# Kernel tuning notes

Hardware: AMD Instinct MI355X
Metric: run time of the kernel (lower is better)

Reference implementation:

```python
import jax, jax.numpy as jnp
import numpy as np

N = 50000
LAMBDA_MAX = 2.0  # PyG default for sym normalization
EPS = 1e-5


def _edge_norm(src, dst, num_nodes):
    # PyG ChebConv.__norm__ with normalization='sym', edge_weight=None:
    # remove self loops, L = I - D^{-1/2} A D^{-1/2}, scale 2/lambda_max, add -1 self loops.
    w = jnp.where(src != dst, 1.0, 0.0)  # remove self loops
    deg = jax.ops.segment_sum(w, src, num_segments=num_nodes)
    dinv = jnp.where(deg > 0, jax.lax.rsqrt(jnp.maximum(deg, 1e-12)), 0.0)
    w_norm = -(2.0 / LAMBDA_MAX) * dinv[src] * w * dinv[dst]  # off-diagonal of scaled L
    diag = (2.0 / LAMBDA_MAX) * 1.0 - 1.0  # scalar diagonal (0.0 when lambda_max=2)
    return w_norm, diag


def _cheb_conv(x, src, dst, w_norm, diag, Ws, b, num_nodes):
    # out = sum_k T_k(L_hat) x @ W_k + b, via Chebyshev recurrence.
    def prop(h):
        msg = w_norm[:, None] * h[src]                       # [E, d]
        return jax.ops.segment_sum(msg, dst, num_segments=num_nodes) + diag * h

    K = Ws.shape[0]
    Tx0 = x
    out = Tx0 @ Ws[0]
    Tx1 = prop(x)
    out = out + Tx1 @ Ws[1]
    for k in range(2, K):
        Tx2 = 2.0 * prop(Tx1) - Tx0
        out = out + Tx2 @ Ws[k]
        Tx0, Tx1 = Tx1, Tx2
    return out + b


def _layernorm(h, g, bt):
    mu = jnp.mean(h, axis=-1, keepdims=True)
    var = jnp.mean(jnp.square(h - mu), axis=-1, keepdims=True)
    return (h - mu) * jax.lax.rsqrt(var + EPS) * g + bt


def setup_inputs() -> dict:
    key = jax.random.key(0)
    ks = jax.random.split(key, 4)
    x = jax.random.normal(ks[0], (N, 128), dtype=jnp.float32)
    edge_index = jax.random.randint(ks[1], (2, 800000), 0, N, dtype=jnp.int64)
    W1 = jax.random.normal(ks[2], (3, 128, 256), dtype=jnp.float32) * 0.05
    W2 = jax.random.normal(ks[3], (3, 256, 128), dtype=jnp.float32) * 0.05
    return {
        "x": x, "edge_index": edge_index,
        "W1": W1, "b1": jnp.zeros((256,), jnp.float32),
        "g1": jnp.ones((256,), jnp.float32), "bt1": jnp.zeros((256,), jnp.float32),
        "W2": W2, "b2": jnp.zeros((128,), jnp.float32),
        "g2": jnp.ones((128,), jnp.float32), "bt2": jnp.zeros((128,), jnp.float32),
    }


def reference(x, edge_index, W1, b1, g1, bt1, W2, b2, g2, bt2):
    src, dst = edge_index[0], edge_index[1]
    w_norm, diag = _edge_norm(src, dst, N)
    h = _cheb_conv(x, src, dst, w_norm, diag, W1, b1, N)
    h = jax.nn.relu(_layernorm(h, g1, bt1))  # dropout p=0 / eval -> identity
    h = _cheb_conv(h, src, dst, w_norm, diag, W2, b2, N)
    h = jax.nn.relu(_layernorm(h, g2, bt2))
    return h
```

## Files before the change

kernel.cpp:

```cpp
#include <hip/hip_runtime.h>

#define N_NODES 50000
#define NRANGE 8
#define RNG 6400
#define TOTR (NRANGE * RNG)
#define NCHUNK 32

using f32x4  = __attribute__((ext_vector_type(4))) float;
using bf16x8 = __attribute__((ext_vector_type(8))) __bf16;

__device__ __forceinline__ unsigned short f2bf(float f) {
    unsigned int b = __float_as_uint(f);
    unsigned int r = (b + 0x7FFFu + ((b >> 16) & 1u)) >> 16;
    return (unsigned short)r;
}
__device__ __forceinline__ float bf_lo(unsigned int u) { return __uint_as_float(u << 16); }
__device__ __forceinline__ float bf_hi(unsigned int u) { return __uint_as_float(u & 0xFFFF0000u); }
__device__ __forceinline__ unsigned int packbf(float x, float y) {
    return ((unsigned int)f2bf(y) << 16) | f2bf(x);
}


__global__ void cvt_bf_kernel(const float* __restrict__ in, unsigned short* __restrict__ out, size_t n4) {
    size_t i = (size_t)blockIdx.x * blockDim.x + threadIdx.x;
    if (i < n4) {
        float4 v = *reinterpret_cast<const float4*>(in + i * 4);
        ushort4 o;
        o.x = f2bf(v.x); o.y = f2bf(v.y); o.z = f2bf(v.z); o.w = f2bf(v.w);
        *reinterpret_cast<ushort4*>(out + i * 4) = o;
    }
}

__global__ void wtrans1_kernel(const float* __restrict__ W, unsigned short* __restrict__ Bt) {
    int i = blockIdx.x * blockDim.x + threadIdx.x;
    if (i < 3 * 128 * 256) {
        int c = i % 256;
        int kg = i / 256;
        Bt[(size_t)c * 384 + kg] = f2bf(W[(size_t)kg * 256 + c]);
    }
}

__global__ void wtrans2_kernel(const float* __restrict__ W, unsigned short* __restrict__ Btc) {
    int i = blockIdx.x * blockDim.x + threadIdx.x;
    if (i < 384 * 256) {
        int k = i % 256;
        int cc = i / 256;
        int seg = cc >> 7, c = cc & 127;
        float v;
        if (seg == 0)      v = W[(size_t)k * 128 + c] - W[(size_t)(2 * 256 + k) * 128 + c];
        else if (seg == 1) v = W[(size_t)(256 + k) * 128 + c];
        else               v = 2.0f * W[(size_t)(2 * 256 + k) * 128 + c];
        Btc[(size_t)cc * 256 + k] = f2bf(v);
    }
}


__global__ __launch_bounds__(1024) void hist_priv_kernel(
        const int* __restrict__ src, const int* __restrict__ dst, int E, int chunk,
        int* __restrict__ pd, int* __restrict__ pc) {
    __shared__ int lhS[RNG];
    __shared__ int lhD[RNG];
    int r = blockIdx.x & (NRANGE - 1);
    int c = blockIdx.x >> 3;
    int lo = r * RNG;
    for (int i = threadIdx.x; i < RNG; i += 1024) { lhS[i] = 0; lhD[i] = 0; }
    __syncthreads();
    int e0 = c * chunk, e1 = min(e0 + chunk, E);
    for (int e = e0 + threadIdx.x; e < e1; e += 1024) {
        int s = src[e], d = dst[e];
        if (s != d) {
            unsigned int sr = (unsigned int)(s - lo);
            unsigned int dr = (unsigned int)(d - lo);
            if (sr < RNG) atomicAdd(&lhS[sr], 1);
            if (dr < RNG) atomicAdd(&lhD[dr], 1);
        }
    }
    __syncthreads();
    int base = c * TOTR + lo;
    for (int i = threadIdx.x; i < RNG; i += 1024) {
        pd[base + i] = lhS[i];
        pc[base + i] = lhD[i];
    }
}

__global__ void reduce_chunks_kernel(int* __restrict__ pd, int* __restrict__ pc,
                                     float* __restrict__ dinv, int* __restrict__ cnt, int n) {
    int i = blockIdx.x * blockDim.x + threadIdx.x;
    if (i >= TOTR) return;
    int degs = 0;
#pragma unroll 8
    for (int c = 0; c < NCHUNK; ++c) degs += pd[c * TOTR + i];
    int run = 0;
#pragma unroll 8
    for (int c = 0; c < NCHUNK; ++c) {
        int v = pc[c * TOTR + i];
        pc[c * TOTR + i] = run;
        run += v;
    }
    if (i < n) {
        dinv[i] = degs > 0 ? rsqrtf((float)degs) : 0.0f;
        cnt[i] = run;
    }
}


__global__ __launch_bounds__(1024) void scan1_kernel(const int* __restrict__ cnt,
                                                     int* __restrict__ excl,
                                                     int* __restrict__ bsum, int n) {
    __shared__ int wsum[16];
    int tid = threadIdx.x, lane = tid & 63, wid = tid >> 6;
    int i = blockIdx.x * 1024 + tid;
    int v = (i < n) ? cnt[i] : 0;
    int x = v;
#pragma unroll
    for (int o = 1; o < 64; o <<= 1) { int y = __shfl_up(x, o); if (lane >= o) x += y; }
    if (lane == 63) wsum[wid] = x;
    __syncthreads();
    if (tid < 16) {
        int s = wsum[tid];
#pragma unroll
        for (int o = 1; o < 16; o <<= 1) { int y = __shfl_up(s, o); if (tid >= o) s += y; }
        wsum[tid] = s;
    }
    __syncthreads();
    int base = (wid > 0 ? wsum[wid - 1] : 0);
    if (i < n) excl[i] = base + x - v;
    if (tid == 0) bsum[blockIdx.x] = wsum[15];
}

__global__ void scan2_kernel(int* __restrict__ bsum, int nb) {
    int t = threadIdx.x;
    int v = (t < nb) ? bsum[t] : 0;
    int x = v;
#pragma unroll
    for (int o = 1; o < 64; o <<= 1) { int y = __shfl_up(x, o); if (t >= o) x += y; }
    if (t < nb) bsum[t] = x - v;
}

__global__ __launch_bounds__(1024) void scan3_kernel(const int* __restrict__ excl,
                                                     const int* __restrict__ bsum,
                                                     const int* __restrict__ cnt,
                                                     int* __restrict__ rowptr, int n) {
    int i = blockIdx.x * 1024 + threadIdx.x;
    if (i < n) {
        int rp = excl[i] + bsum[blockIdx.x];
        rowptr[i] = rp;
        if (i == n - 1) rowptr[n] = rp + cnt[i];
    }
}

__global__ __launch_bounds__(1024) void csr_place_kernel(
        const int* __restrict__ src, const int* __restrict__ dst, int E, int chunk,
        const int* __restrict__ pc, const int* __restrict__ rowptr,
        const float* __restrict__ dinv,
        int* __restrict__ csr_src, float* __restrict__ csr_w, int n) {
    __shared__ int cur[RNG];
    __shared__ float dloc[RNG];
    int r = blockIdx.x & (NRANGE - 1);
    int c = blockIdx.x >> 3;
    int lo = r * RNG;
    for (int i = threadIdx.x; i < RNG; i += 1024) {
        int node = lo + i;
        if (node < n) {
            cur[i] = rowptr[node] + pc[c * TOTR + node];
            dloc[i] = dinv[node];
        }
    }
    __syncthreads();
    int e0 = c * chunk, e1 = min(e0 + chunk, E);
    for (int e = e0 + threadIdx.x; e < e1; e += 1024) {
        int s = src[e], d = dst[e];
        unsigned int dr = (unsigned int)(d - lo);
        if (s != d && dr < RNG) {
            int pos = atomicAdd(&cur[dr], 1);
            csr_src[pos] = s;
            csr_w[pos] = -dinv[s] * dloc[dr];
        }
    }
}


__global__ void prop_kernel(const unsigned int* __restrict__ H, int hs,
                            const int* __restrict__ rowptr,
                            const int* __restrict__ csr_src,
                            const float* __restrict__ csr_w,
                            const unsigned int* __restrict__ add, int as_,
                            float scale, float coef,
                            unsigned int* __restrict__ out, int n) {
    int wib = threadIdx.x >> 6;
    int lane = threadIdx.x & 63;
    int node = blockIdx.x * (blockDim.x >> 6) + wib;
    if (node >= n) return;

    float ax = 0.0f, ay = 0.0f;
    int beg = rowptr[node], end = rowptr[node + 1];
    int i = beg;
    for (; i + 4 <= end; i += 4) {
        int s0 = csr_src[i], s1 = csr_src[i + 1], s2 = csr_src[i + 2], s3 = csr_src[i + 3];
        float w0 = csr_w[i], w1 = csr_w[i + 1], w2 = csr_w[i + 2], w3 = csr_w[i + 3];
        unsigned int u0 = H[(size_t)s0 * hs + lane];
        unsigned int u1 = H[(size_t)s1 * hs + lane];
        unsigned int u2 = H[(size_t)s2 * hs + lane];
        unsigned int u3 = H[(size_t)s3 * hs + lane];
        ax += w0 * bf_lo(u0) + w1 * bf_lo(u1) + w2 * bf_lo(u2) + w3 * bf_lo(u3);
        ay += w0 * bf_hi(u0) + w1 * bf_hi(u1) + w2 * bf_hi(u2) + w3 * bf_hi(u3);
    }
    for (; i < end; ++i) {
        int s0 = csr_src[i];
        float w0 = csr_w[i];
        unsigned int u0 = H[(size_t)s0 * hs + lane];
        ax += w0 * bf_lo(u0);
        ay += w0 * bf_hi(u0);
    }

    float vx = scale * ax, vy = scale * ay;
    if (add) {
        unsigned int au = add[(size_t)node * as_ + lane];
        vx += coef * bf_lo(au);
        vy += coef * bf_hi(au);
    }
    out[(size_t)node * 64 + lane] = packbf(vx, vy);
}

__global__ void prop_ln_kernel(const unsigned int* __restrict__ V,
                               const int* __restrict__ rowptr,
                               const int* __restrict__ csr_src,
                               const float* __restrict__ csr_w,
                               const unsigned int* __restrict__ U0,
                               const float* __restrict__ b,
                               const float* __restrict__ g,
                               const float* __restrict__ bt,
                               float* __restrict__ out, int n) {
    int wib = threadIdx.x >> 6;
    int lane = threadIdx.x & 63;
    int node = blockIdx.x * (blockDim.x >> 6) + wib;
    if (node >= n) return;

    float ax = 0.0f, ay = 0.0f;
    int beg = rowptr[node], end = rowptr[node + 1];
    int i = beg;
    for (; i + 4 <= end; i += 4) {
        int s0 = csr_src[i], s1 = csr_src[i + 1], s2 = csr_src[i + 2], s3 = csr_src[i + 3];
        float w0 = csr_w[i], w1 = csr_w[i + 1], w2 = csr_w[i + 2], w3 = csr_w[i + 3];
        unsigned int u0 = V[(size_t)s0 * 64 + lane];
        unsigned int u1 = V[(size_t)s1 * 64 + lane];
        unsigned int u2 = V[(size_t)s2 * 64 + lane];
        unsigned int u3 = V[(size_t)s3 * 64 + lane];
        ax += w0 * bf_lo(u0) + w1 * bf_lo(u1) + w2 * bf_lo(u2) + w3 * bf_lo(u3);
        ay += w0 * bf_hi(u0) + w1 * bf_hi(u1) + w2 * bf_hi(u2) + w3 * bf_hi(u3);
    }
    for (; i < end; ++i) {
        int s0 = csr_src[i];
        float w0 = csr_w[i];
        unsigned int u0 = V[(size_t)s0 * 64 + lane];
        ax += w0 * bf_lo(u0);
        ay += w0 * bf_hi(u0);
    }

    unsigned int au = U0[(size_t)node * 192 + lane];
    float px = ax + bf_lo(au) + b[2 * lane];
    float py = ay + bf_hi(au) + b[2 * lane + 1];

    float s = px + py;
#pragma unroll
    for (int o = 1; o < 64; o <<= 1) s += __shfl_xor(s, o);
    float mu = s * (1.0f / 128.0f);
    float dx = px - mu, dy = py - mu;
    float q = dx * dx + dy * dy;
#pragma unroll
    for (int o = 1; o < 64; o <<= 1) q += __shfl_xor(q, o);
    float rs = rsqrtf(q * (1.0f / 128.0f) + 1e-5f);

    float yx = dx * rs * g[2 * lane] + bt[2 * lane];
    float yy = dy * rs * g[2 * lane + 1] + bt[2 * lane + 1];
    yx = yx > 0.0f ? yx : 0.0f;
    yy = yy > 0.0f ? yy : 0.0f;
    float2 o2 = make_float2(yx, yy);
    *reinterpret_cast<float2*>(out + (size_t)node * 128 + 2 * lane) = o2;
}


__global__ __launch_bounds__(256) void gemm1_ln_kernel(
        const unsigned short* __restrict__ A0, const unsigned short* __restrict__ A1,
        const unsigned short* __restrict__ A2, const unsigned short* __restrict__ Bt,
        const float* __restrict__ bias, const float* __restrict__ g,
        const float* __restrict__ bt, unsigned short* __restrict__ Hout, int N) {
    __shared__ __align__(16) unsigned short As[64][40];
    __shared__ __align__(16) unsigned short Bs[256][40];
    __shared__ float redS[4][64];
    __shared__ float redQ[4][64];

    int row0 = blockIdx.x * 64;
    int tid = threadIdx.x;
    int lane = tid & 63;
    int wave = tid >> 6;
    int wc = wave * 64;

    f32x4 acc[4][4];
#pragma unroll
    for (int i = 0; i < 4; ++i)
#pragma unroll
        for (int j = 0; j < 4; ++j) acc[i][j] = (f32x4)0.0f;

    int srow = tid >> 2;
    int sch = (tid & 3) * 8;

    for (int ks = 0; ks < 12; ++ks) {
        int kg = ks * 32;
        int seg = kg >> 7;
        int kk = kg & 127;
        const unsigned short* Aseg = (seg == 0) ? A0 : (seg == 1 ? A1 : A2);
        {
            int gr = row0 + srow;
            uint4 v = make_uint4(0u, 0u, 0u, 0u);
            if (gr < N) v = *reinterpret_cast<const uint4*>(Aseg + (size_t)gr * 128 + kk + sch);
            *reinterpret_cast<uint4*>(&As[srow][sch]) = v;
        }
#pragma unroll
        for (int p = 0; p < 4; ++p) {
            int rr = p * 64 + srow;
            uint4 v = *reinterpret_cast<const uint4*>(Bt + (size_t)rr * 384 + kg + sch);
            *reinterpret_cast<uint4*>(&Bs[rr][sch]) = v;
        }
        __syncthreads();

        int fr = lane & 15;
        int kh = (lane >> 4) * 8;
        bf16x8 af[4], bfr[4];
#pragma unroll
        for (int i = 0; i < 4; ++i)
            af[i] = *reinterpret_cast<const bf16x8*>(&As[i * 16 + fr][kh]);
#pragma unroll
        for (int j = 0; j < 4; ++j)
            bfr[j] = *reinterpret_cast<const bf16x8*>(&Bs[wc + j * 16 + fr][kh]);
#pragma unroll
        for (int i = 0; i < 4; ++i)
#pragma unroll
            for (int j = 0; j < 4; ++j)
                acc[i][j] = __builtin_amdgcn_mfma_f32_16x16x32_bf16(af[i], bfr[j], acc[i][j], 0, 0, 0);
        __syncthreads();
    }

    int fc = lane & 15;
    int fq = lane >> 4;
    float bcol[4], gcol[4], btcol[4];
#pragma unroll
    for (int j = 0; j < 4; ++j) {
        int c = wc + j * 16 + fc;
        bcol[j] = bias[c];
        gcol[j] = g[c];
        btcol[j] = bt[c];
    }
#pragma unroll
    for (int i = 0; i < 4; ++i)
#pragma unroll
        for (int j = 0; j < 4; ++j)
#pragma unroll
            for (int v = 0; v < 4; ++v) acc[i][j][v] += bcol[j];

#pragma unroll
    for (int i = 0; i < 4; ++i) {
#pragma unroll
        for (int v = 0; v < 4; ++v) {
            float s = 0.0f, q = 0.0f;
#pragma unroll
            for (int j = 0; j < 4; ++j) {
                float val = acc[i][j][v];
                s += val;
                q += val * val;
            }
#pragma unroll
            for (int o = 1; o < 16; o <<= 1) {
                s += __shfl_xor(s, o);
                q += __shfl_xor(q, o);
            }
            if (fc == 0) {
                int r = i * 16 + fq * 4 + v;
                redS[wave][r] = s;
                redQ[wave][r] = q;
            }
        }
    }
    __syncthreads();

#pragma unroll
    for (int i = 0; i < 4; ++i) {
#pragma unroll
        for (int v = 0; v < 4; ++v) {
            int r = i * 16 + fq * 4 + v;
            float S = redS[0][r] + redS[1][r] + redS[2][r] + redS[3][r];
            float Q = redQ[0][r] + redQ[1][r] + redQ[2][r] + redQ[3][r];
            float mu = S * (1.0f / 256.0f);
            float var = Q * (1.0f / 256.0f) - mu * mu;
            float rsg = rsqrtf(var + 1e-5f);
            int gr = row0 + r;
            if (gr < N) {
#pragma unroll
                for (int j = 0; j < 4; ++j) {
                    float y = (acc[i][j][v] - mu) * rsg * gcol[j] + btcol[j];
                    y = y > 0.0f ? y : 0.0f;
                    Hout[(size_t)gr * 256 + wc + j * 16 + fc] = f2bf(y);
                }
            }
        }
    }
}


__global__ __launch_bounds__(256) void gemm2_kernel(
        const unsigned short* __restrict__ A, const unsigned short* __restrict__ Btc,
        unsigned short* __restrict__ U, int N, int ncol) {
    __shared__ __align__(16) unsigned short As[64][40];
    __shared__ __align__(16) unsigned short Bs[128][40];

    int nwg = gridDim.x;
    int q = nwg >> 3, r = nwg & 7;
    int xcd = blockIdx.x & 7, idx = blockIdx.x >> 3;
    int wgid = (xcd < r ? xcd * (q + 1) : r * (q + 1) + (xcd - r) * q) + idx;

    int row0 = (wgid / ncol) * 64;
    int col0 = (wgid % ncol) * 128;

    int tid = threadIdx.x;
    int lane = tid & 63;
    int wave = tid >> 6;
    int wc = wave * 32;

    f32x4 acc[4][2];
#pragma unroll
    for (int i = 0; i < 4; ++i)
#pragma unroll
        for (int j = 0; j < 2; ++j) acc[i][j] = (f32x4)0.0f;

    int srow = tid >> 2;
    int sch = (tid & 3) * 8;

    for (int ks = 0; ks < 8; ++ks) {
        int kg = ks * 32;
        {
            int gr = row0 + srow;
            uint4 v = make_uint4(0u, 0u, 0u, 0u);
            if (gr < N) v = *reinterpret_cast<const uint4*>(A + (size_t)gr * 256 + kg + sch);
            *reinterpret_cast<uint4*>(&As[srow][sch]) = v;
        }
#pragma unroll
        for (int p = 0; p < 2; ++p) {
            int rr = p * 64 + srow;
            uint4 v = *reinterpret_cast<const uint4*>(Btc + (size_t)(col0 + rr) * 256 + kg + sch);
            *reinterpret_cast<uint4*>(&Bs[rr][sch]) = v;
        }
        __syncthreads();

        int fr = lane & 15;
        int kh = (lane >> 4) * 8;
        bf16x8 af[4], bfr[2];
#pragma unroll
        for (int i = 0; i < 4; ++i)
            af[i] = *reinterpret_cast<const bf16x8*>(&As[i * 16 + fr][kh]);
#pragma unroll
        for (int j = 0; j < 2; ++j)
            bfr[j] = *reinterpret_cast<const bf16x8*>(&Bs[wc + j * 16 + fr][kh]);
#pragma unroll
        for (int i = 0; i < 4; ++i)
#pragma unroll
            for (int j = 0; j < 2; ++j)
                acc[i][j] = __builtin_amdgcn_mfma_f32_16x16x32_bf16(af[i], bfr[j], acc[i][j], 0, 0, 0);
        __syncthreads();
    }

    int fc = lane & 15;
    int frr = (lane >> 4) * 4;
#pragma unroll
    for (int i = 0; i < 4; ++i) {
#pragma unroll
        for (int v = 0; v < 4; ++v) {
            int gr = row0 + i * 16 + frr + v;
            if (gr < N) {
#pragma unroll
                for (int j = 0; j < 2; ++j) {
                    int gc = col0 + wc + j * 16 + fc;
                    U[(size_t)gr * 384 + gc] = f2bf(acc[i][j][v]);
                }
            }
        }
    }
}


extern "C" void kernel_launch(void* const* d_in, const int* in_sizes, int n_in,
                              void* d_out, int out_size, void* d_ws, size_t ws_size,
                              hipStream_t stream) {
    const int N = N_NODES;
    const float* x  = (const float*)d_in[0];
    const int*  ei  = (const int*)d_in[1];
    const float* W1 = (const float*)d_in[2];
    const float* b1 = (const float*)d_in[3];
    const float* g1 = (const float*)d_in[4];
    const float* bt1 = (const float*)d_in[5];
    const float* W2 = (const float*)d_in[6];
    const float* b2 = (const float*)d_in[7];
    const float* g2 = (const float*)d_in[8];
    const float* bt2 = (const float*)d_in[9];
    float* out = (float*)d_out;

    const int E = in_sizes[1] / 2;
    const int* src = ei;
    const int* dst = ei + E;
    const int chunk = (E + NCHUNK - 1) / NCHUNK;

    char* w = (char*)d_ws;
    auto alloc = [&](size_t bytes) { char* p = w; w += (bytes + 255) & ~(size_t)255; return p; };
    int* pd      = (int*)alloc((size_t)NCHUNK * TOTR * 4);
    int* pc      = (int*)alloc((size_t)NCHUNK * TOTR * 4);
    int* cnt     = (int*)alloc((size_t)N * 4);
    int* excl    = (int*)alloc((size_t)N * 4);
    int* bsum    = (int*)alloc(64 * 4);
    int* rowptr  = (int*)alloc((size_t)(N + 1) * 4);
    int* csr_src = (int*)alloc((size_t)E * 4);
    float* dinv  = (float*)alloc((size_t)N * 4);
    float* csr_w = (float*)alloc((size_t)E * 4);
    unsigned short* xb  = (unsigned short*)alloc((size_t)N * 128 * 2);
    unsigned short* T1  = (unsigned short*)alloc((size_t)N * 128 * 2);
    unsigned short* T2  = (unsigned short*)alloc((size_t)N * 128 * 2);
    unsigned short* h1b = (unsigned short*)alloc((size_t)N * 256 * 2);
    unsigned short* U   = (unsigned short*)alloc((size_t)N * 384 * 2);
    unsigned short* V   = (unsigned short*)alloc((size_t)N * 128 * 2);
    unsigned short* Bt1 = (unsigned short*)alloc((size_t)256 * 384 * 2);
    unsigned short* Btc = (unsigned short*)alloc((size_t)384 * 256 * 2);
    (void)ws_size;

    const int TPB = 256;
    const int NB = (N + 1023) / 1024;

    hipLaunchKernelGGL(hist_priv_kernel, dim3(NCHUNK * NRANGE), dim3(1024), 0, stream,
                       src, dst, E, chunk, pd, pc);
    hipLaunchKernelGGL(reduce_chunks_kernel, dim3((TOTR + TPB - 1) / TPB), dim3(TPB), 0, stream,
                       pd, pc, dinv, cnt, N);
    hipLaunchKernelGGL(scan1_kernel, dim3(NB), dim3(1024), 0, stream, cnt, excl, bsum, N);
    hipLaunchKernelGGL(scan2_kernel, dim3(1), dim3(64), 0, stream, bsum, NB);
    hipLaunchKernelGGL(scan3_kernel, dim3(NB), dim3(1024), 0, stream, excl, bsum, cnt, rowptr, N);
    hipLaunchKernelGGL(csr_place_kernel, dim3(NCHUNK * NRANGE), dim3(1024), 0, stream,
                       src, dst, E, chunk, pc, rowptr, dinv, csr_src, csr_w, N);
    hipLaunchKernelGGL(cvt_bf_kernel, dim3((N * 128 / 4 + TPB - 1) / TPB), dim3(TPB), 0, stream,
                       x, xb, (size_t)N * 128 / 4);
    hipLaunchKernelGGL(wtrans1_kernel, dim3((3 * 128 * 256 + TPB - 1) / TPB), dim3(TPB), 0, stream, W1, Bt1);
    hipLaunchKernelGGL(wtrans2_kernel, dim3((384 * 256 + TPB - 1) / TPB), dim3(TPB), 0, stream, W2, Btc);

    const int gridW = (N + 3) / 4;

    hipLaunchKernelGGL(prop_kernel, dim3(gridW), dim3(TPB), 0, stream,
                       (const unsigned int*)xb, 64, rowptr, csr_src, csr_w,
                       (const unsigned int*)nullptr, 0, 1.0f, 0.0f,
                       (unsigned int*)T1, N);
    hipLaunchKernelGGL(prop_kernel, dim3(gridW), dim3(TPB), 0, stream,
                       (const unsigned int*)T1, 64, rowptr, csr_src, csr_w,
                       (const unsigned int*)xb, 64, 2.0f, -1.0f,
                       (unsigned int*)T2, N);
    hipLaunchKernelGGL(gemm1_ln_kernel, dim3((N + 63) / 64), dim3(256), 0, stream,
                       xb, T1, T2, Bt1, b1, g1, bt1, h1b, N);

    {
        int nrow = (N + 63) / 64, ncol = 3;
        hipLaunchKernelGGL(gemm2_kernel, dim3(nrow * ncol), dim3(256), 0, stream,
                           h1b, Btc, U, N, ncol);
    }
    hipLaunchKernelGGL(prop_kernel, dim3(gridW), dim3(TPB), 0, stream,
                       (const unsigned int*)U + 128, 192, rowptr, csr_src, csr_w,
                       (const unsigned int*)U + 64, 192, 1.0f, 1.0f,
                       (unsigned int*)V, N);
    hipLaunchKernelGGL(prop_ln_kernel, dim3(gridW), dim3(TPB), 0, stream,
                       (const unsigned int*)V, rowptr, csr_src, csr_w,
                       (const unsigned int*)U, b2, g2, bt2, out, N);
}
```

Before: 281.6 us.

## Interleave CSR src/weight into int2 and double-buffer GEMM shared tiles

The CSR source indices and edge weights are stored interleaved as int2, so each prop kernel gets both with one 8-byte load per edge instead of two separate loads. Both GEMM kernels now double-buffer their LDS tiles, prefetching the next K-slice into registers while MFMAs run on the current buffer, and drop one barrier per iteration. Out-of-range A rows are clamped to the last row rather than zero-filled, which only changes output rows that are never stored. Shared memory per block doubles for the GEMM tiles, and more registers are live for the prefetch.

```diff
diff --git a/kernel.cpp b/kernel.cpp
--- a/kernel.cpp
+++ b/kernel.cpp
@@ -153,7 +153,7 @@
         const int* __restrict__ src, const int* __restrict__ dst, int E, int chunk,
         const int* __restrict__ pc, const int* __restrict__ rowptr,
         const float* __restrict__ dinv,
-        int* __restrict__ csr_src, float* __restrict__ csr_w, int n) {
+        int2* __restrict__ csr, int n) {
     __shared__ int cur[RNG];
     __shared__ float dloc[RNG];
     int r = blockIdx.x & (NRANGE - 1);
@@ -173,8 +173,7 @@
         unsigned int dr = (unsigned int)(d - lo);
         if (s != d && dr < RNG) {
             int pos = atomicAdd(&cur[dr], 1);
-            csr_src[pos] = s;
-            csr_w[pos] = -dinv[s] * dloc[dr];
+            csr[pos] = make_int2(s, __float_as_int(-dinv[s] * dloc[dr]));
         }
     }
 }
@@ -182,8 +181,7 @@
 
 __global__ void prop_kernel(const unsigned int* __restrict__ H, int hs,
                             const int* __restrict__ rowptr,
-                            const int* __restrict__ csr_src,
-                            const float* __restrict__ csr_w,
+                            const int2* __restrict__ csr,
                             const unsigned int* __restrict__ add, int as_,
                             float scale, float coef,
                             unsigned int* __restrict__ out, int n) {
@@ -196,19 +194,20 @@
     int beg = rowptr[node], end = rowptr[node + 1];
     int i = beg;
     for (; i + 4 <= end; i += 4) {
-        int s0 = csr_src[i], s1 = csr_src[i + 1], s2 = csr_src[i + 2], s3 = csr_src[i + 3];
-        float w0 = csr_w[i], w1 = csr_w[i + 1], w2 = csr_w[i + 2], w3 = csr_w[i + 3];
-        unsigned int u0 = H[(size_t)s0 * hs + lane];
-        unsigned int u1 = H[(size_t)s1 * hs + lane];
-        unsigned int u2 = H[(size_t)s2 * hs + lane];
-        unsigned int u3 = H[(size_t)s3 * hs + lane];
+        int2 e0 = csr[i], e1 = csr[i + 1], e2 = csr[i + 2], e3 = csr[i + 3];
+        unsigned int u0 = H[(size_t)e0.x * hs + lane];
+        unsigned int u1 = H[(size_t)e1.x * hs + lane];
+        unsigned int u2 = H[(size_t)e2.x * hs + lane];
+        unsigned int u3 = H[(size_t)e3.x * hs + lane];
+        float w0 = __int_as_float(e0.y), w1 = __int_as_float(e1.y);
+        float w2 = __int_as_float(e2.y), w3 = __int_as_float(e3.y);
         ax += w0 * bf_lo(u0) + w1 * bf_lo(u1) + w2 * bf_lo(u2) + w3 * bf_lo(u3);
         ay += w0 * bf_hi(u0) + w1 * bf_hi(u1) + w2 * bf_hi(u2) + w3 * bf_hi(u3);
     }
     for (; i < end; ++i) {
-        int s0 = csr_src[i];
-        float w0 = csr_w[i];
-        unsigned int u0 = H[(size_t)s0 * hs + lane];
+        int2 e0 = csr[i];
+        unsigned int u0 = H[(size_t)e0.x * hs + lane];
+        float w0 = __int_as_float(e0.y);
         ax += w0 * bf_lo(u0);
         ay += w0 * bf_hi(u0);
     }
@@ -224,8 +223,7 @@
 
 __global__ void prop_ln_kernel(const unsigned int* __restrict__ V,
                                const int* __restrict__ rowptr,
-                               const int* __restrict__ csr_src,
-                               const float* __restrict__ csr_w,
+                               const int2* __restrict__ csr,
                                const unsigned int* __restrict__ U0,
                                const float* __restrict__ b,
                                const float* __restrict__ g,
@@ -240,19 +238,20 @@
     int beg = rowptr[node], end = rowptr[node + 1];
     int i = beg;
     for (; i + 4 <= end; i += 4) {
-        int s0 = csr_src[i], s1 = csr_src[i + 1], s2 = csr_src[i + 2], s3 = csr_src[i + 3];
-        float w0 = csr_w[i], w1 = csr_w[i + 1], w2 = csr_w[i + 2], w3 = csr_w[i + 3];
-        unsigned int u0 = V[(size_t)s0 * 64 + lane];
-        unsigned int u1 = V[(size_t)s1 * 64 + lane];
-        unsigned int u2 = V[(size_t)s2 * 64 + lane];
-        unsigned int u3 = V[(size_t)s3 * 64 + lane];
+        int2 e0 = csr[i], e1 = csr[i + 1], e2 = csr[i + 2], e3 = csr[i + 3];
+        unsigned int u0 = V[(size_t)e0.x * 64 + lane];
+        unsigned int u1 = V[(size_t)e1.x * 64 + lane];
+        unsigned int u2 = V[(size_t)e2.x * 64 + lane];
+        unsigned int u3 = V[(size_t)e3.x * 64 + lane];
+        float w0 = __int_as_float(e0.y), w1 = __int_as_float(e1.y);
+        float w2 = __int_as_float(e2.y), w3 = __int_as_float(e3.y);
         ax += w0 * bf_lo(u0) + w1 * bf_lo(u1) + w2 * bf_lo(u2) + w3 * bf_lo(u3);
         ay += w0 * bf_hi(u0) + w1 * bf_hi(u1) + w2 * bf_hi(u2) + w3 * bf_hi(u3);
     }
     for (; i < end; ++i) {
-        int s0 = csr_src[i];
-        float w0 = csr_w[i];
-        unsigned int u0 = V[(size_t)s0 * 64 + lane];
+        int2 e0 = csr[i];
+        unsigned int u0 = V[(size_t)e0.x * 64 + lane];
+        float w0 = __int_as_float(e0.y);
         ax += w0 * bf_lo(u0);
         ay += w0 * bf_hi(u0);
     }
@@ -285,8 +284,8 @@
         const unsigned short* __restrict__ A2, const unsigned short* __restrict__ Bt,
         const float* __restrict__ bias, const float* __restrict__ g,
         const float* __restrict__ bt, unsigned short* __restrict__ Hout, int N) {
-    __shared__ __align__(16) unsigned short As[64][40];
-    __shared__ __align__(16) unsigned short Bs[256][40];
+    __shared__ __align__(16) unsigned short As[2][64][40];
+    __shared__ __align__(16) unsigned short Bs[2][256][40];
     __shared__ float redS[4][64];
     __shared__ float redQ[4][64];
 
@@ -304,41 +303,47 @@
 
     int srow = tid >> 2;
     int sch = (tid & 3) * 8;
-
-    for (int ks = 0; ks < 12; ++ks) {
+    int gra = min(row0 + srow, N - 1);
+
+    uint4 ra, rb0, rb1, rb2, rb3;
+    auto issue = [&](int ks) {
         int kg = ks * 32;
         int seg = kg >> 7;
         int kk = kg & 127;
         const unsigned short* Aseg = (seg == 0) ? A0 : (seg == 1 ? A1 : A2);
-        {
-            int gr = row0 + srow;
-            uint4 v = make_uint4(0u, 0u, 0u, 0u);
-            if (gr < N) v = *reinterpret_cast<const uint4*>(Aseg + (size_t)gr * 128 + kk + sch);
-            *reinterpret_cast<uint4*>(&As[srow][sch]) = v;
-        }
-#pragma unroll
-        for (int p = 0; p < 4; ++p) {
-            int rr = p * 64 + srow;
-            uint4 v = *reinterpret_cast<const uint4*>(Bt + (size_t)rr * 384 + kg + sch);
-            *reinterpret_cast<uint4*>(&Bs[rr][sch]) = v;
-        }
+        ra = *reinterpret_cast<const uint4*>(Aseg + (size_t)gra * 128 + kk + sch);
+        const unsigned short* bp = Bt + (size_t)srow * 384 + kg + sch;
+        rb0 = *reinterpret_cast<const uint4*>(bp);
+        rb1 = *reinterpret_cast<const uint4*>(bp + (size_t)64 * 384);
+        rb2 = *reinterpret_cast<const uint4*>(bp + (size_t)128 * 384);
+        rb3 = *reinterpret_cast<const uint4*>(bp + (size_t)192 * 384);
+    };
+
+    issue(0);
+    for (int ks = 0; ks < 12; ++ks) {
+        int cb = ks & 1;
+        *reinterpret_cast<uint4*>(&As[cb][srow][sch]) = ra;
+        *reinterpret_cast<uint4*>(&Bs[cb][srow][sch]) = rb0;
+        *reinterpret_cast<uint4*>(&Bs[cb][64 + srow][sch]) = rb1;
+        *reinterpret_cast<uint4*>(&Bs[cb][128 + srow][sch]) = rb2;
+        *reinterpret_cast<uint4*>(&Bs[cb][192 + srow][sch]) = rb3;
         __syncthreads();
+        if (ks < 11) issue(ks + 1);
 
         int fr = lane & 15;
         int kh = (lane >> 4) * 8;
         bf16x8 af[4], bfr[4];
 #pragma unroll
         for (int i = 0; i < 4; ++i)
-            af[i] = *reinterpret_cast<const bf16x8*>(&As[i * 16 + fr][kh]);
+            af[i] = *reinterpret_cast<const bf16x8*>(&As[cb][i * 16 + fr][kh]);
 #pragma unroll
         for (int j = 0; j < 4; ++j)
-            bfr[j] = *reinterpret_cast<const bf16x8*>(&Bs[wc + j * 16 + fr][kh]);
+            bfr[j] = *reinterpret_cast<const bf16x8*>(&Bs[cb][wc + j * 16 + fr][kh]);
 #pragma unroll
         for (int i = 0; i < 4; ++i)
 #pragma unroll
             for (int j = 0; j < 4; ++j)
                 acc[i][j] = __builtin_amdgcn_mfma_f32_16x16x32_bf16(af[i], bfr[j], acc[i][j], 0, 0, 0);
-        __syncthreads();
     }
 
     int fc = lane & 15;
@@ -410,8 +415,8 @@
 __global__ __launch_bounds__(256) void gemm2_kernel(
         const unsigned short* __restrict__ A, const unsigned short* __restrict__ Btc,
         unsigned short* __restrict__ U, int N, int ncol) {
-    __shared__ __align__(16) unsigned short As[64][40];
-    __shared__ __align__(16) unsigned short Bs[128][40];
+    __shared__ __align__(16) unsigned short As[2][64][40];
+    __shared__ __align__(16) unsigned short Bs[2][128][40];
 
     int nwg = gridDim.x;
     int q = nwg >> 3, r = nwg & 7;
@@ -434,38 +439,40 @@
 
     int srow = tid >> 2;
     int sch = (tid & 3) * 8;
-
+    int gra = min(row0 + srow, N - 1);
+
+    uint4 ra, rb0, rb1;
+    auto issue = [&](int ks) {
+        int kg = ks * 32;
+        ra = *reinterpret_cast<const uint4*>(A + (size_t)gra * 256 + kg + sch);
+        const unsigned short* bp = Btc + (size_t)(col0 + srow) * 256 + kg + sch;
+        rb0 = *reinterpret_cast<const uint4*>(bp);
+        rb1 = *reinterpret_cast<const uint4*>(bp + (size_t)64 * 256);
+    };
+
+    issue(0);
     for (int ks = 0; ks < 8; ++ks) {
-        int kg = ks * 32;
-        {
-            int gr = row0 + srow;
-            uint4 v = make_uint4(0u, 0u, 0u, 0u);
-            if (gr < N) v = *reinterpret_cast<const uint4*>(A + (size_t)gr * 256 + kg + sch);
-            *reinterpret_cast<uint4*>(&As[srow][sch]) = v;
-        }
-#pragma unroll
-        for (int p = 0; p < 2; ++p) {
-            int rr = p * 64 + srow;
-            uint4 v = *reinterpret_cast<const uint4*>(Btc + (size_t)(col0 + rr) * 256 + kg + sch);
-            *reinterpret_cast<uint4*>(&Bs[rr][sch]) = v;
-        }
+        int cb = ks & 1;
+        *reinterpret_cast<uint4*>(&As[cb][srow][sch]) = ra;
+        *reinterpret_cast<uint4*>(&Bs[cb][srow][sch]) = rb0;
+        *reinterpret_cast<uint4*>(&Bs[cb][64 + srow][sch]) = rb1;
         __syncthreads();
+        if (ks < 7) issue(ks + 1);
 
         int fr = lane & 15;
         int kh = (lane >> 4) * 8;
         bf16x8 af[4], bfr[2];
 #pragma unroll
         for (int i = 0; i < 4; ++i)
-            af[i] = *reinterpret_cast<const bf16x8*>(&As[i * 16 + fr][kh]);
+            af[i] = *reinterpret_cast<const bf16x8*>(&As[cb][i * 16 + fr][kh]);
 #pragma unroll
         for (int j = 0; j < 2; ++j)
-            bfr[j] = *reinterpret_cast<const bf16x8*>(&Bs[wc + j * 16 + fr][kh]);
+            bfr[j] = *reinterpret_cast<const bf16x8*>(&Bs[cb][wc + j * 16 + fr][kh]);
 #pragma unroll
         for (int i = 0; i < 4; ++i)
 #pragma unroll
             for (int j = 0; j < 2; ++j)
                 acc[i][j] = __builtin_amdgcn_mfma_f32_16x16x32_bf16(af[i], bfr[j], acc[i][j], 0, 0, 0);
-        __syncthreads();
     }
 
     int fc = lane & 15;
@@ -516,9 +523,8 @@
     int* excl    = (int*)alloc((size_t)N * 4);
     int* bsum    = (int*)alloc(64 * 4);
     int* rowptr  = (int*)alloc((size_t)(N + 1) * 4);
-    int* csr_src = (int*)alloc((size_t)E * 4);
+    int2* csr    = (int2*)alloc((size_t)E * 8);
     float* dinv  = (float*)alloc((size_t)N * 4);
-    float* csr_w = (float*)alloc((size_t)E * 4);
     unsigned short* xb  = (unsigned short*)alloc((size_t)N * 128 * 2);
     unsigned short* T1  = (unsigned short*)alloc((size_t)N * 128 * 2);
     unsigned short* T2  = (unsigned short*)alloc((size_t)N * 128 * 2);
@@ -540,7 +546,7 @@
     hipLaunchKernelGGL(scan2_kernel, dim3(1), dim3(64), 0, stream, bsum, NB);
     hipLaunchKernelGGL(scan3_kernel, dim3(NB), dim3(1024), 0, stream, excl, bsum, cnt, rowptr, N);
     hipLaunchKernelGGL(csr_place_kernel, dim3(NCHUNK * NRANGE), dim3(1024), 0, stream,
-                       src, dst, E, chunk, pc, rowptr, dinv, csr_src, csr_w, N);
+                       src, dst, E, chunk, pc, rowptr, dinv, csr, N);
     hipLaunchKernelGGL(cvt_bf_kernel, dim3((N * 128 / 4 + TPB - 1) / TPB), dim3(TPB), 0, stream,
                        x, xb, (size_t)N * 128 / 4);
     hipLaunchKernelGGL(wtrans1_kernel, dim3((3 * 128 * 256 + TPB - 1) / TPB), dim3(TPB), 0, stream, W1, Bt1);
@@ -549,11 +555,11 @@
     const int gridW = (N + 3) / 4;
 
     hipLaunchKernelGGL(prop_kernel, dim3(gridW), dim3(TPB), 0, stream,
-                       (const unsigned int*)xb, 64, rowptr, csr_src, csr_w,
+                       (const unsigned int*)xb, 64, rowptr, csr,
                        (const unsigned int*)nullptr, 0, 1.0f, 0.0f,
                        (unsigned int*)T1, N);
     hipLaunchKernelGGL(prop_kernel, dim3(gridW), dim3(TPB), 0, stream,
-                       (const unsigned int*)T1, 64, rowptr, csr_src, csr_w,
+                       (const unsigned int*)T1, 64, rowptr, csr,
                        (const unsigned int*)xb, 64, 2.0f, -1.0f,
                        (unsigned int*)T2, N);
     hipLaunchKernelGGL(gemm1_ln_kernel, dim3((N + 63) / 64), dim3(256), 0, stream,
@@ -565,10 +571,10 @@
                            h1b, Btc, U, N, ncol);
     }
     hipLaunchKernelGGL(prop_kernel, dim3(gridW), dim3(TPB), 0, stream,
-                       (const unsigned int*)U + 128, 192, rowptr, csr_src, csr_w,
+                       (const unsigned int*)U + 128, 192, rowptr, csr,
                        (const unsigned int*)U + 64, 192, 1.0f, 1.0f,
                        (unsigned int*)V, N);
     hipLaunchKernelGGL(prop_ln_kernel, dim3(gridW), dim3(TPB), 0, stream,
-                       (const unsigned int*)V, rowptr, csr_src, csr_w,
+                       (const unsigned int*)V, rowptr, csr,
                        (const unsigned int*)U, b2, g2, bt2, out, N);
 }
```

After: 278.0 us. No clear change (-1.3%).
